# Kernel optimization log

Hardware: AMD Instinct MI355X
Metric: run time of the kernel (lower is better)

Reference implementation:

```python
import jax, jax.numpy as jnp
import numpy as np

CUTOFF = 10.0
NUM_RADIAL = 64  # RPEncoding(num_radial=64)
NHEAD = 8
D_MODEL = 512
N_SPH = 9  # lmax=2 -> 1+3+5 real spherical harmonics


def _sph_harm_l2(dirs):
    # real spherical harmonics up to l=2 on unit vectors; dirs: [..., 3]
    x, y, z = dirs[..., 0], dirs[..., 1], dirs[..., 2]
    c0 = 0.28209479177387814
    c1 = 0.4886025119029199
    c2 = 1.0925484305920792
    c20 = 0.31539156525252005
    c22 = 0.5462742152960396
    return jnp.stack([
        jnp.full_like(x, c0),
        c1 * y, c1 * z, c1 * x,
        c2 * x * y, c2 * y * z, c20 * (3.0 * z * z - 1.0), c2 * x * z,
        c22 * (x * x - y * y),
    ], axis=-1)  # [..., 9]


def _rbf(d):
    # gaussian radial basis with cosine cutoff envelope; d: [...]
    centers = jnp.linspace(0.0, CUTOFF, NUM_RADIAL)
    width = CUTOFF / NUM_RADIAL
    g = jnp.exp(-((d[..., None] - centers) ** 2) / (2.0 * width * width))
    env = 0.5 * (jnp.cos(jnp.pi * jnp.clip(d / CUTOFF, 0.0, 1.0)) + 1.0)
    return g * env[..., None]  # [..., NUM_RADIAL]


def _layer_norm(x, g, b, eps=1e-5):
    mu = jnp.mean(x, axis=-1, keepdims=True)
    var = jnp.mean(jnp.square(x - mu), axis=-1, keepdims=True)
    return (x - mu) * jax.lax.rsqrt(var + eps) * g + b


def setup_inputs() -> dict:
    key = jax.random.key(0)
    ks = jax.random.split(key, 8)
    B, L, D, F = 2, 256, D_MODEL, NUM_RADIAL * N_SPH
    src = jax.random.normal(ks[0], (B, L, D), dtype=jnp.float32)
    rel_diss = jax.random.uniform(ks[1], (B, L, L), dtype=jnp.float32) * CUTOFF
    dirs = jax.random.normal(ks[2], (B, L, L, 3), dtype=jnp.float32)
    rel_dirs = dirs / (jnp.linalg.norm(dirs, axis=-1, keepdims=True) + 1e-8)
    s = 0.02
    return {
        'src': src,
        'rel_diss': rel_diss,
        'rel_dirs': rel_dirs,
        'rp_w': jax.random.normal(ks[3], (F, D), dtype=jnp.float32) * s,
        'rp_b': jnp.zeros((D,), dtype=jnp.float32),
        'w1': jax.random.normal(ks[4], (D, 4 * D), dtype=jnp.float32) * s,
        'b1': jnp.zeros((4 * D,), dtype=jnp.float32),
        'w2': jax.random.normal(ks[5], (4 * D, D), dtype=jnp.float32) * s,
        'b2': jnp.zeros((D,), dtype=jnp.float32),
        'gamma1': jnp.ones((D,), dtype=jnp.float32),
        'beta1': jnp.zeros((D,), dtype=jnp.float32),
        'gamma2': jnp.ones((D,), dtype=jnp.float32),
        'beta2': jnp.zeros((D,), dtype=jnp.float32),
    }


def reference(src, rel_diss, rel_dirs, rp_w, rp_b, w1, b1, w2, b2,
              gamma1, beta1, gamma2, beta2):
    B, L, D = src.shape
    H, Dh = NHEAD, D // NHEAD

    # relative-position embedding: RBF(dist) outer sph-harm(dir) -> [B,L,L,576]
    rbf = _rbf(rel_diss)                 # [B,L,L,R]
    sph = _sph_harm_l2(rel_dirs)         # [B,L,L,S]
    rp_raw = (sph[..., :, None] * rbf[..., None, :]).reshape(B, L, L, -1)
    rp = jnp.einsum('blmf,fd->blmd', rp_raw, rp_w) + rp_b  # [B,L,L,D]
    rp = rp.reshape(B, L, L, H, Dh)

    # manual attention path (raw src as q/k/v, no projections, as in source)
    qh = src.reshape(B, L, H, Dh)
    rp_scores = jnp.einsum('blhd,blmhd->bhlm', qh, rp)
    base = jnp.einsum('blhd,bmhd->bhlm', qh / np.sqrt(Dh).astype(np.float32), qh)
    attn_w = jax.nn.softmax(base + rp_scores, axis=-1)
    attn = jnp.einsum('bhlm,bmhd->blhd', attn_w, qh).reshape(B, L, D)

    x = _layer_norm(src + attn, gamma1, beta1)
    h = jax.nn.leaky_relu(x @ w1 + b1, negative_slope=0.01)
    x = _layer_norm(x + h @ w2 + b2, gamma2, beta2)
    return x
```

## Files before the change

### kernel.cpp

```cpp
#include <hip/hip_runtime.h>

#define NB 2
#define NL 256
#define ND 512
#define NH 8
#define NDH 64
#define NR 64
#define NS 9
#define NF 576
#define NHS 72
#define WQROW 4608
#define RWIN 12

typedef __attribute__((ext_vector_type(8))) short bf16x8;
typedef __attribute__((ext_vector_type(4))) float f32x4;

__device__ __forceinline__ ushort f2b(float f) {
    union { float f; unsigned u; } c; c.f = f;
    unsigned u = c.u;
    return (ushort)((u + 0x7FFF + ((u >> 16) & 1)) >> 16);
}

__device__ __forceinline__ float block_sum4(float v, float* s_red) {
    #pragma unroll
    for (int off = 32; off; off >>= 1) v += __shfl_xor(v, off, 64);
    __syncthreads();
    if ((threadIdx.x & 63) == 0) s_red[threadIdx.x >> 6] = v;
    __syncthreads();
    return s_red[0] + s_red[1] + s_red[2] + s_red[3];
}

__device__ __forceinline__ float block_sum8(float v, float* s_red) {
    #pragma unroll
    for (int off = 32; off; off >>= 1) v += __shfl_xor(v, off, 64);
    __syncthreads();
    if ((threadIdx.x & 63) == 0) s_red[threadIdx.x >> 6] = v;
    __syncthreads();
    return ((s_red[0] + s_red[1]) + (s_red[2] + s_red[3])) +
           ((s_red[4] + s_red[5]) + (s_red[6] + s_red[7]));
}

__global__ __launch_bounds__(256, 4) void k_pre(const float* __restrict__ src,
                                                const float* __restrict__ rp_w,
                                                const float* __restrict__ w1,
                                                const float* __restrict__ w2,
                                                float* __restrict__ Wq,
                                                float* __restrict__ sbuf,
                                                ushort* __restrict__ w1t,
                                                ushort* __restrict__ w2t) {
    __shared__ __align__(16) char raw[26368];
    int bi = blockIdx.x;
    int t = threadIdx.x;

    if (bi < 512) {
        const float* in;
        ushort* out;
        int K, N, bx, by;
        if (bi < 256) { in = w1; out = w1t; K = 512; N = 2048; bx = bi & 31; by = bi >> 5; }
        else { int id = bi - 256; in = w2; out = w2t; K = 2048; N = 512; bx = id & 7; by = id >> 3; }
        float (*tile)[65] = (float(*)[65])raw;
        int n0 = bx * 64, k0 = by * 64;
        int r = t >> 4, c4 = (t & 15) * 4;
        #pragma unroll
        for (int i = 0; i < 4; ++i) {
            int kk = i * 16 + r;
            float4 v = *(const float4*)(in + (size_t)(k0 + kk) * N + n0 + c4);
            tile[kk][c4 + 0] = v.x;
            tile[kk][c4 + 1] = v.y;
            tile[kk][c4 + 2] = v.z;
            tile[kk][c4 + 3] = v.w;
        }
        __syncthreads();
        int rr = t >> 2, cq = (t & 3) * 16;
        ushort buf[16];
        #pragma unroll
        for (int j = 0; j < 16; ++j) buf[j] = f2b(tile[cq + j][rr]);
        ushort* op = out + (size_t)(n0 + rr) * K + k0 + cq;
        *(uint4*)(op) = *(uint4*)&buf[0];
        *(uint4*)(op + 8) = *(uint4*)&buf[8];
    } else if (bi < 1024) {
        int id = bi - 512;
        int rt = id & 63, h = id >> 6;
        float (*s_src)[64] = (float(*)[64])raw;
        float* s_B = (float*)(raw + 2048);
        int r0 = rt * 8;
        {
            int sr = t >> 5;
            int sc = (t & 31) * 2;
            *(float2*)&s_src[sr][sc] =
                *(const float2*)(src + (size_t)(r0 + sr) * ND + h * 64 + sc);
        }
        int ff = t & 63;
        int g  = t >> 6;
        int lr = t >> 2;
        int lq = t & 3;
        const float* bsrc = rp_w + h * 64;
        #pragma unroll 1
        for (int s = 0; s < NS; ++s) {
            __syncthreads();
            #pragma unroll
            for (int i = 0; i < 4; ++i) {
                int slot = i * 4 + lq;
                float4 v = *(const float4*)(bsrc + (size_t)(s * 64 + lr) * ND + slot * 4);
                int sw = slot ^ (lr & 7);
                *(float4*)&s_B[lr * 64 + sw * 4] = v;
            }
            __syncthreads();
            float a0 = 0.f, a1 = 0.f;
            #pragma unroll
            for (int d4 = 0; d4 < 16; ++d4) {
                int sw = d4 ^ (ff & 7);
                float4 bv = *(const float4*)&s_B[ff * 64 + sw * 4];
                float4 s0 = *(const float4*)&s_src[2 * g][d4 * 4];
                float4 s1 = *(const float4*)&s_src[2 * g + 1][d4 * 4];
                a0 = fmaf(bv.x, s0.x, a0);
                a0 = fmaf(bv.y, s0.y, a0);
                a0 = fmaf(bv.z, s0.z, a0);
                a0 = fmaf(bv.w, s0.w, a0);
                a1 = fmaf(bv.x, s1.x, a1);
                a1 = fmaf(bv.y, s1.y, a1);
                a1 = fmaf(bv.z, s1.z, a1);
                a1 = fmaf(bv.w, s1.w, a1);
            }
            Wq[(size_t)(r0 + 2 * g) * WQROW + ff * NHS + h * NS + s] = a0;
            Wq[(size_t)(r0 + 2 * g + 1) * WQROW + ff * NHS + h * NS + s] = a1;
        }
    } else {
        int id = bi - 1024;
        int mt = id & 3, lt = (id >> 2) & 7, bh = id >> 5;
        int b = bh >> 3, h = bh & 7;
        int m0 = mt * 64, l0 = lt * 32;
        float (*s_A)[68] = (float(*)[68])raw;
        float (*s_B)[68] = (float(*)[68])(raw + 8704);
        #pragma unroll
        for (int i = 0; i < 2; ++i) {
            int idx = i * 256 + t;
            int row = idx >> 4, c4 = idx & 15;
            float4 v = *(const float4*)(src + (size_t)(b * NL + l0 + row) * ND + h * 64 + c4 * 4);
            *(float4*)&s_A[row][c4 * 4] = v;
        }
        {
            int mr = t >> 2, qd = t & 3;
            const float* kp = src + (size_t)(b * NL + m0 + mr) * ND + h * 64 + qd * 16;
            #pragma unroll
            for (int q = 0; q < 4; ++q) {
                float4 v = *(const float4*)(kp + q * 4);
                int d = qd * 16 + q * 4;
                s_B[d + 0][mr] = v.x;
                s_B[d + 1][mr] = v.y;
                s_B[d + 2][mr] = v.z;
                s_B[d + 3][mr] = v.w;
            }
        }
        __syncthreads();
        int tx = t & 15, ty = t >> 4;
        int ty2 = ty * 2;
        float acc[2][4] = {};
        #pragma unroll
        for (int d = 0; d < 64; ++d) {
            float a0 = s_A[ty2][d];
            float a1 = s_A[ty2 + 1][d];
            float4 bv = *(const float4*)&s_B[d][tx * 4];
            acc[0][0] = fmaf(a0, bv.x, acc[0][0]);
            acc[0][1] = fmaf(a0, bv.y, acc[0][1]);
            acc[0][2] = fmaf(a0, bv.z, acc[0][2]);
            acc[0][3] = fmaf(a0, bv.w, acc[0][3]);
            acc[1][0] = fmaf(a1, bv.x, acc[1][0]);
            acc[1][1] = fmaf(a1, bv.y, acc[1][1]);
            acc[1][2] = fmaf(a1, bv.z, acc[1][2]);
            acc[1][3] = fmaf(a1, bv.w, acc[1][3]);
        }
        #pragma unroll
        for (int i = 0; i < 2; ++i) {
            size_t off = ((size_t)bh * NL + l0 + ty2 + i) * NL + m0 + tx * 4;
            *(float4*)(sbuf + off) = make_float4(acc[i][0] * 0.125f, acc[i][1] * 0.125f,
                                                 acc[i][2] * 0.125f, acc[i][3] * 0.125f);
        }
    }
}

__global__ __launch_bounds__(512, 4) void k2_fused(const float* __restrict__ src,
                                                   const float* __restrict__ rel_diss,
                                                   const float* __restrict__ rel_dirs,
                                                   const float* __restrict__ Wq,
                                                   const float* __restrict__ sbuf,
                                                   const float* __restrict__ gamma1,
                                                   const float* __restrict__ beta1,
                                                   float* __restrict__ x1buf,
                                                   ushort* __restrict__ x1bf) {
    int row = blockIdx.x;
    int b = row >> 8;
    int l = row & 255;
    int t = threadIdx.x;
    int m = t & 255;
    int hg = t >> 8;
    __shared__ float s_wq[64][76];
    __shared__ float s_l[NH][NL];
    __shared__ float s_red[8];

    const float* wrow = Wq + (size_t)row * WQROW;
    #pragma unroll
    for (int i = 0; i < 9; ++i) {
        int flat = i * 512 + t;
        int r = flat / 72, c = flat - 72 * r;
        s_wq[r][c] = wrow[flat];
    }

    float dist = rel_diss[(size_t)row * NL + m];
    const float* dirp = rel_dirs + ((size_t)row * NL + m) * 3;
    float x = dirp[0], y = dirp[1], z = dirp[2];
    float tcl = fminf(fmaxf(dist * 0.1f, 0.f), 1.f);
    float env = 0.5f * (__cosf(3.14159265358979f * tcl) + 1.f);
    int rc = (int)floorf(dist * 6.3f + 0.5f);
    int rlo = min(max(rc - 6, 0), NR - RWIN);
    float sph[NS];
    sph[0] = 0.28209479177387814f * env;
    sph[1] = 0.4886025119029199f * y * env;
    sph[2] = 0.4886025119029199f * z * env;
    sph[3] = 0.4886025119029199f * x * env;
    sph[4] = 1.0925484305920792f * x * y * env;
    sph[5] = 1.0925484305920792f * y * z * env;
    sph[6] = 0.31539156525252005f * (3.f * z * z - 1.f) * env;
    sph[7] = 1.0925484305920792f * x * z * env;
    sph[8] = 0.5462742152960396f * (x * x - y * y) * env;

    __syncthreads();

    float acc[36];
    #pragma unroll
    for (int i = 0; i < 36; ++i) acc[i] = 0.f;
    #pragma unroll 4
    for (int rw = 0; rw < RWIN; ++rw) {
        int r = rlo + rw;
        float df = dist - r * (10.f / 63.f);
        float rbf = __expf(-df * df * 20.48f);
        const float* wp = &s_wq[r][hg * 36];
        #pragma unroll
        for (int q = 0; q < 9; ++q) {
            float4 w = *(const float4*)(wp + q * 4);
            acc[q * 4 + 0] = fmaf(w.x, rbf, acc[q * 4 + 0]);
            acc[q * 4 + 1] = fmaf(w.y, rbf, acc[q * 4 + 1]);
            acc[q * 4 + 2] = fmaf(w.z, rbf, acc[q * 4 + 2]);
            acc[q * 4 + 3] = fmaf(w.w, rbf, acc[q * 4 + 3]);
        }
    }

    const float* sb = sbuf + (((size_t)(b * NH + hg * 4) * NL) + l) * NL + m;
    #pragma unroll
    for (int hh = 0; hh < 4; ++hh) {
        float sc = 0.f;
        #pragma unroll
        for (int s = 0; s < NS; ++s) sc = fmaf(sph[s], acc[hh * NS + s], sc);
        s_l[hg * 4 + hh][m] = sc + sb[(size_t)hh * NL * NL];
    }
    __syncthreads();

    int wv = t >> 6, lane = t & 63;
    {
        float v0 = s_l[wv][lane], v1 = s_l[wv][lane + 64];
        float v2 = s_l[wv][lane + 128], v3 = s_l[wv][lane + 192];
        float mx = fmaxf(fmaxf(v0, v1), fmaxf(v2, v3));
        #pragma unroll
        for (int off = 32; off; off >>= 1) mx = fmaxf(mx, __shfl_xor(mx, off, 64));
        float p0 = __expf(v0 - mx), p1 = __expf(v1 - mx);
        float p2 = __expf(v2 - mx), p3 = __expf(v3 - mx);
        float sm = p0 + p1 + p2 + p3;
        #pragma unroll
        for (int off = 32; off; off >>= 1) sm += __shfl_xor(sm, off, 64);
        float inv = 1.f / sm;
        s_l[wv][lane] = p0 * inv;
        s_l[wv][lane + 64] = p1 * inv;
        s_l[wv][lane + 128] = p2 * inv;
        s_l[wv][lane + 192] = p3 * inv;
    }
    __syncthreads();

    int d = t;
    int h0 = t >> 6;
    float a0 = 0.f, a1 = 0.f, a2 = 0.f, a3 = 0.f;
    const float* vbase = src + (size_t)b * NL * ND + d;
    #pragma unroll 2
    for (int mm = 0; mm < NL; mm += 4) {
        float4 wv4 = *(const float4*)&s_l[h0][mm];
        a0 = fmaf(wv4.x, vbase[(size_t)(mm + 0) * ND], a0);
        a1 = fmaf(wv4.y, vbase[(size_t)(mm + 1) * ND], a1);
        a2 = fmaf(wv4.z, vbase[(size_t)(mm + 2) * ND], a2);
        a3 = fmaf(wv4.w, vbase[(size_t)(mm + 3) * ND], a3);
    }
    float av = (a0 + a1) + (a2 + a3);

    float x0 = src[(size_t)row * ND + d] + av;
    float mu = block_sum8(x0, s_red) * (1.f / 512.f);
    float e0 = x0 - mu;
    float var = block_sum8(e0 * e0, s_red) * (1.f / 512.f);
    float rs = rsqrtf(var + 1e-5f);
    float o = e0 * rs * gamma1[d] + beta1[d];
    x1buf[(size_t)row * ND + d] = o;
    x1bf[(size_t)row * ND + d] = f2b(o);
}

__global__ __launch_bounds__(256) void k3_mfma(const ushort* __restrict__ A,
                                               const ushort* __restrict__ Bt,
                                               const float* __restrict__ bias,
                                               ushort* __restrict__ C) {
    const int K = 512, N = 2048;
    int n0 = blockIdx.x * 64, m0 = blockIdx.y * 64;
    int t = threadIdx.x;
    int w = t >> 6, l = t & 63;
    __shared__ ushort As[64][40];
    __shared__ ushort Bs[64][40];
    f32x4 acc0 = {0.f, 0.f, 0.f, 0.f}, acc1 = acc0, acc2 = acc0, acc3 = acc0;
    int sr = t >> 2, sq = (t & 3) * 8;
    const ushort* Ap = A + (size_t)(m0 + sr) * K + sq;
    const ushort* Bp = Bt + (size_t)(n0 + sr) * K + sq;
    int lr = l & 15, lk = (l >> 4) * 8;
    for (int k0 = 0; k0 < K; k0 += 32) {
        uint4 av = *(const uint4*)(Ap + k0);
        uint4 bv = *(const uint4*)(Bp + k0);
        __syncthreads();
        *(uint4*)&As[sr][sq] = av;
        *(uint4*)&Bs[sr][sq] = bv;
        __syncthreads();
        bf16x8 af = *(const bf16x8*)&As[w * 16 + lr][lk];
        bf16x8 b0 = *(const bf16x8*)&Bs[0 * 16 + lr][lk];
        bf16x8 b1 = *(const bf16x8*)&Bs[1 * 16 + lr][lk];
        bf16x8 b2 = *(const bf16x8*)&Bs[2 * 16 + lr][lk];
        bf16x8 b3 = *(const bf16x8*)&Bs[3 * 16 + lr][lk];
        acc0 = __builtin_amdgcn_mfma_f32_16x16x32_bf16(af, b0, acc0, 0, 0, 0);
        acc1 = __builtin_amdgcn_mfma_f32_16x16x32_bf16(af, b1, acc1, 0, 0, 0);
        acc2 = __builtin_amdgcn_mfma_f32_16x16x32_bf16(af, b2, acc2, 0, 0, 0);
        acc3 = __builtin_amdgcn_mfma_f32_16x16x32_bf16(af, b3, acc3, 0, 0, 0);
    }
    int rbase = m0 + w * 16 + (l >> 4) * 4;
    #pragma unroll
    for (int e = 0; e < 4; ++e) {
        int row = rbase + e;
        float v;
        int col0 = n0 + lr;
        v = acc0[e] + bias[col0];
        C[(size_t)row * N + col0] = f2b(v >= 0.f ? v : 0.01f * v);
        v = acc1[e] + bias[col0 + 16];
        C[(size_t)row * N + col0 + 16] = f2b(v >= 0.f ? v : 0.01f * v);
        v = acc2[e] + bias[col0 + 32];
        C[(size_t)row * N + col0 + 32] = f2b(v >= 0.f ? v : 0.01f * v);
        v = acc3[e] + bias[col0 + 48];
        C[(size_t)row * N + col0 + 48] = f2b(v >= 0.f ? v : 0.01f * v);
    }
}

__global__ __launch_bounds__(256) void k4_mfma(const ushort* __restrict__ A,
                                               const ushort* __restrict__ Bt,
                                               float* __restrict__ Cp) {
    const int K = 2048, N = 512;
    int n0 = blockIdx.x * 64, m0 = blockIdx.y * 64;
    int ks = blockIdx.z;
    int t = threadIdx.x;
    int w = t >> 6, l = t & 63;
    __shared__ ushort As[64][40];
    __shared__ ushort Bs[64][40];
    f32x4 acc0 = {0.f, 0.f, 0.f, 0.f}, acc1 = acc0, acc2 = acc0, acc3 = acc0;
    int sr = t >> 2, sq = (t & 3) * 8;
    const ushort* Ap = A + (size_t)(m0 + sr) * K + ks * 512 + sq;
    const ushort* Bp = Bt + (size_t)(n0 + sr) * K + ks * 512 + sq;
    int lr = l & 15, lk = (l >> 4) * 8;
    for (int k0 = 0; k0 < 512; k0 += 32) {
        uint4 av = *(const uint4*)(Ap + k0);
        uint4 bv = *(const uint4*)(Bp + k0);
        __syncthreads();
        *(uint4*)&As[sr][sq] = av;
        *(uint4*)&Bs[sr][sq] = bv;
        __syncthreads();
        bf16x8 af = *(const bf16x8*)&As[w * 16 + lr][lk];
        bf16x8 b0 = *(const bf16x8*)&Bs[0 * 16 + lr][lk];
        bf16x8 b1 = *(const bf16x8*)&Bs[1 * 16 + lr][lk];
        bf16x8 b2 = *(const bf16x8*)&Bs[2 * 16 + lr][lk];
        bf16x8 b3 = *(const bf16x8*)&Bs[3 * 16 + lr][lk];
        acc0 = __builtin_amdgcn_mfma_f32_16x16x32_bf16(af, b0, acc0, 0, 0, 0);
        acc1 = __builtin_amdgcn_mfma_f32_16x16x32_bf16(af, b1, acc1, 0, 0, 0);
        acc2 = __builtin_amdgcn_mfma_f32_16x16x32_bf16(af, b2, acc2, 0, 0, 0);
        acc3 = __builtin_amdgcn_mfma_f32_16x16x32_bf16(af, b3, acc3, 0, 0, 0);
    }
    float* out = Cp + ((size_t)ks << 18);
    int rbase = m0 + w * 16 + (l >> 4) * 4;
    #pragma unroll
    for (int e = 0; e < 4; ++e) {
        int row = rbase + e;
        int col0 = n0 + lr;
        out[(size_t)row * N + col0] = acc0[e];
        out[(size_t)row * N + col0 + 16] = acc1[e];
        out[(size_t)row * N + col0 + 32] = acc2[e];
        out[(size_t)row * N + col0 + 48] = acc3[e];
    }
}

__global__ __launch_bounds__(256) void k5_final(const float* __restrict__ x1buf,
                                                const float* __restrict__ zpart,
                                                const float* __restrict__ b2,
                                                const float* __restrict__ gamma2,
                                                const float* __restrict__ beta2,
                                                float* __restrict__ out) {
    int row = blockIdx.x;
    int t = threadIdx.x;
    int d0 = t * 2;
    __shared__ float s_red[8];
    size_t off = (size_t)row * ND + d0;
    float2 v = *(const float2*)(x1buf + off);
    float2 bb = *(const float2*)(b2 + d0);
    float z0 = v.x + bb.x, z1 = v.y + bb.y;
    #pragma unroll
    for (int ks = 0; ks < 4; ++ks) {
        float2 p = *(const float2*)(zpart + ((size_t)ks << 18) + off);
        z0 += p.x;
        z1 += p.y;
    }
    float mu = block_sum4(z0 + z1, s_red) * (1.f / 512.f);
    float e0 = z0 - mu, e1 = z1 - mu;
    float var = block_sum4(e0 * e0 + e1 * e1, s_red) * (1.f / 512.f);
    float rs = rsqrtf(var + 1e-5f);
    float2 g = *(const float2*)(gamma2 + d0), be = *(const float2*)(beta2 + d0);
    *(float2*)(out + off) = make_float2(e0 * rs * g.x + be.x, e1 * rs * g.y + be.y);
}

extern "C" void kernel_launch(void* const* d_in, const int* in_sizes, int n_in,
                              void* d_out, int out_size, void* d_ws, size_t ws_size,
                              hipStream_t stream) {
    const float* src      = (const float*)d_in[0];
    const float* rel_diss = (const float*)d_in[1];
    const float* rel_dirs = (const float*)d_in[2];
    const float* rp_w     = (const float*)d_in[3];
    const float* w1  = (const float*)d_in[5];
    const float* b1  = (const float*)d_in[6];
    const float* w2  = (const float*)d_in[7];
    const float* b2  = (const float*)d_in[8];
    const float* g1  = (const float*)d_in[9];
    const float* be1 = (const float*)d_in[10];
    const float* g2  = (const float*)d_in[11];
    const float* be2 = (const float*)d_in[12];
    float* out = (float*)d_out;

    float* ws = (float*)d_ws;
    float* x1buf = ws;
    float* sbuf  = x1buf + 262144;
    float* zpart = sbuf + 1048576;
    float* Wq    = zpart + 1048576;
    ushort* w1t  = (ushort*)(Wq + WQROW * 512);
    ushort* w2t  = w1t + 1048576;
    ushort* x1bf = w2t + 1048576;
    ushort* hbf  = x1bf + 262144;

    k_pre<<<1536, 256, 0, stream>>>(src, rp_w, w1, w2, Wq, sbuf, w1t, w2t);
    k2_fused<<<512, 512, 0, stream>>>(src, rel_diss, rel_dirs, Wq, sbuf,
                                      g1, be1, x1buf, x1bf);
    k3_mfma<<<dim3(32, 8), 256, 0, stream>>>(x1bf, w1t, b1, hbf);
    k4_mfma<<<dim3(8, 8, 4), 256, 0, stream>>>(hbf, w2t, zpart);
    k5_final<<<512, 256, 0, stream>>>(x1buf, zpart, b2, g2, be2, out);
}
```

Before: 66.65 us.

## Fuse final layernorm into split-K GEMM via last-block counter; vectorize PV

```diff
diff --git a/kernel.cpp b/kernel.cpp
--- a/kernel.cpp
+++ b/kernel.cpp
@@ -4,7 +4,6 @@
 #define NL 256
 #define ND 512
 #define NH 8
-#define NDH 64
 #define NR 64
 #define NS 9
 #define NF 576
@@ -19,15 +18,6 @@
     union { float f; unsigned u; } c; c.f = f;
     unsigned u = c.u;
     return (ushort)((u + 0x7FFF + ((u >> 16) & 1)) >> 16);
-}
-
-__device__ __forceinline__ float block_sum4(float v, float* s_red) {
-    #pragma unroll
-    for (int off = 32; off; off >>= 1) v += __shfl_xor(v, off, 64);
-    __syncthreads();
-    if ((threadIdx.x & 63) == 0) s_red[threadIdx.x >> 6] = v;
-    __syncthreads();
-    return s_red[0] + s_red[1] + s_red[2] + s_red[3];
 }
 
 __device__ __forceinline__ float block_sum8(float v, float* s_red) {
@@ -47,15 +37,15 @@
                                                 float* __restrict__ Wq,
                                                 float* __restrict__ sbuf,
                                                 ushort* __restrict__ w1t,
-                                                ushort* __restrict__ w2t) {
+                                                ushort* __restrict__ w2t,
+                                                unsigned* __restrict__ ctr) {
     __shared__ __align__(16) char raw[26368];
     int bi = blockIdx.x;
     int t = threadIdx.x;
+    if (bi == 0 && t < 8) ctr[t] = 0;
 
     if (bi < 512) {
-        const float* in;
-        ushort* out;
-        int K, N, bx, by;
+        const float* in; ushort* out; int K, N, bx, by;
         if (bi < 256) { in = w1; out = w1t; K = 512; N = 2048; bx = bi & 31; by = bi >> 5; }
         else { int id = bi - 256; in = w2; out = w2t; K = 2048; N = 512; bx = id & 7; by = id >> 3; }
         float (*tile)[65] = (float(*)[65])raw;
@@ -196,6 +186,7 @@
     int hg = t >> 8;
     __shared__ float s_wq[64][76];
     __shared__ float s_l[NH][NL];
+    __shared__ float s_pv[2][ND];
     __shared__ float s_red[8];
 
     const float* wrow = Wq + (size_t)row * WQROW;
@@ -205,7 +196,6 @@
         int r = flat / 72, c = flat - 72 * r;
         s_wq[r][c] = wrow[flat];
     }
-
     float dist = rel_diss[(size_t)row * NL + m];
     const float* dirp = rel_dirs + ((size_t)row * NL + m) * 3;
     float x = dirp[0], y = dirp[1], z = dirp[2];
@@ -223,7 +213,6 @@
     sph[6] = 0.31539156525252005f * (3.f * z * z - 1.f) * env;
     sph[7] = 1.0925484305920792f * x * z * env;
     sph[8] = 0.5462742152960396f * (x * x - y * y) * env;
-
     __syncthreads();
 
     float acc[36];
@@ -244,7 +233,6 @@
             acc[q * 4 + 3] = fmaf(w.w, rbf, acc[q * 4 + 3]);
         }
     }
-
     const float* sb = sbuf + (((size_t)(b * NH + hg * 4) * NL) + l) * NL + m;
     #pragma unroll
     for (int hh = 0; hh < 4; ++hh) {
@@ -275,20 +263,30 @@
     }
     __syncthreads();
 
+    {
+        int p = t & 255, half = t >> 8;
+        int d0 = p * 2;
+        int h0 = p >> 5;
+        float a0 = 0.f, a1 = 0.f, c0 = 0.f, c1 = 0.f;
+        const float* vb = src + (size_t)b * NL * ND + (size_t)(half * 128) * ND + d0;
+        const float* wl = &s_l[h0][half * 128];
+        #pragma unroll 2
+        for (int mm = 0; mm < 128; mm += 2) {
+            float2 w2v = *(const float2*)(wl + mm);
+            float2 v0 = *(const float2*)(vb + (size_t)mm * ND);
+            float2 v1 = *(const float2*)(vb + (size_t)(mm + 1) * ND);
+            a0 = fmaf(w2v.x, v0.x, a0);
+            a1 = fmaf(w2v.x, v0.y, a1);
+            c0 = fmaf(w2v.y, v1.x, c0);
+            c1 = fmaf(w2v.y, v1.y, c1);
+        }
+        s_pv[half][d0] = a0 + c0;
+        s_pv[half][d0 + 1] = a1 + c1;
+    }
+    __syncthreads();
+
     int d = t;
-    int h0 = t >> 6;
-    float a0 = 0.f, a1 = 0.f, a2 = 0.f, a3 = 0.f;
-    const float* vbase = src + (size_t)b * NL * ND + d;
-    #pragma unroll 2
-    for (int mm = 0; mm < NL; mm += 4) {
-        float4 wv4 = *(const float4*)&s_l[h0][mm];
-        a0 = fmaf(wv4.x, vbase[(size_t)(mm + 0) * ND], a0);
-        a1 = fmaf(wv4.y, vbase[(size_t)(mm + 1) * ND], a1);
-        a2 = fmaf(wv4.z, vbase[(size_t)(mm + 2) * ND], a2);
-        a3 = fmaf(wv4.w, vbase[(size_t)(mm + 3) * ND], a3);
-    }
-    float av = (a0 + a1) + (a2 + a3);
-
+    float av = s_pv[0][d] + s_pv[1][d];
     float x0 = src[(size_t)row * ND + d] + av;
     float mu = block_sum8(x0, s_red) * (1.f / 512.f);
     float e0 = x0 - mu;
@@ -323,12 +321,12 @@
         __syncthreads();
         bf16x8 af = *(const bf16x8*)&As[w * 16 + lr][lk];
         bf16x8 b0 = *(const bf16x8*)&Bs[0 * 16 + lr][lk];
-        bf16x8 b1 = *(const bf16x8*)&Bs[1 * 16 + lr][lk];
-        bf16x8 b2 = *(const bf16x8*)&Bs[2 * 16 + lr][lk];
+        bf16x8 b1v = *(const bf16x8*)&Bs[1 * 16 + lr][lk];
+        bf16x8 b2v = *(const bf16x8*)&Bs[2 * 16 + lr][lk];
         bf16x8 b3 = *(const bf16x8*)&Bs[3 * 16 + lr][lk];
         acc0 = __builtin_amdgcn_mfma_f32_16x16x32_bf16(af, b0, acc0, 0, 0, 0);
-        acc1 = __builtin_amdgcn_mfma_f32_16x16x32_bf16(af, b1, acc1, 0, 0, 0);
-        acc2 = __builtin_amdgcn_mfma_f32_16x16x32_bf16(af, b2, acc2, 0, 0, 0);
+        acc1 = __builtin_amdgcn_mfma_f32_16x16x32_bf16(af, b1v, acc1, 0, 0, 0);
+        acc2 = __builtin_amdgcn_mfma_f32_16x16x32_bf16(af, b2v, acc2, 0, 0, 0);
         acc3 = __builtin_amdgcn_mfma_f32_16x16x32_bf16(af, b3, acc3, 0, 0, 0);
     }
     int rbase = m0 + w * 16 + (l >> 4) * 4;
@@ -348,9 +346,15 @@
     }
 }
 
-__global__ __launch_bounds__(256) void k4_mfma(const ushort* __restrict__ A,
-                                               const ushort* __restrict__ Bt,
-                                               float* __restrict__ Cp) {
+__global__ __launch_bounds__(256) void k4_fused(const ushort* __restrict__ A,
+                                                const ushort* __restrict__ Bt,
+                                                float* __restrict__ Cp,
+                                                const float* __restrict__ x1buf,
+                                                const float* __restrict__ b2,
+                                                const float* __restrict__ gamma2,
+                                                const float* __restrict__ beta2,
+                                                float* __restrict__ out,
+                                                unsigned* __restrict__ ctr) {
     const int K = 2048, N = 512;
     int n0 = blockIdx.x * 64, m0 = blockIdx.y * 64;
     int ks = blockIdx.z;
@@ -358,6 +362,7 @@
     int w = t >> 6, l = t & 63;
     __shared__ ushort As[64][40];
     __shared__ ushort Bs[64][40];
+    __shared__ bool s_last;
     f32x4 acc0 = {0.f, 0.f, 0.f, 0.f}, acc1 = acc0, acc2 = acc0, acc3 = acc0;
     int sr = t >> 2, sq = (t & 3) * 8;
     const ushort* Ap = A + (size_t)(m0 + sr) * K + ks * 512 + sq;
@@ -372,53 +377,82 @@
         __syncthreads();
         bf16x8 af = *(const bf16x8*)&As[w * 16 + lr][lk];
         bf16x8 b0 = *(const bf16x8*)&Bs[0 * 16 + lr][lk];
-        bf16x8 b1 = *(const bf16x8*)&Bs[1 * 16 + lr][lk];
-        bf16x8 b2 = *(const bf16x8*)&Bs[2 * 16 + lr][lk];
+        bf16x8 b1v = *(const bf16x8*)&Bs[1 * 16 + lr][lk];
+        bf16x8 b2v = *(const bf16x8*)&Bs[2 * 16 + lr][lk];
         bf16x8 b3 = *(const bf16x8*)&Bs[3 * 16 + lr][lk];
         acc0 = __builtin_amdgcn_mfma_f32_16x16x32_bf16(af, b0, acc0, 0, 0, 0);
-        acc1 = __builtin_amdgcn_mfma_f32_16x16x32_bf16(af, b1, acc1, 0, 0, 0);
-        acc2 = __builtin_amdgcn_mfma_f32_16x16x32_bf16(af, b2, acc2, 0, 0, 0);
+        acc1 = __builtin_amdgcn_mfma_f32_16x16x32_bf16(af, b1v, acc1, 0, 0, 0);
+        acc2 = __builtin_amdgcn_mfma_f32_16x16x32_bf16(af, b2v, acc2, 0, 0, 0);
         acc3 = __builtin_amdgcn_mfma_f32_16x16x32_bf16(af, b3, acc3, 0, 0, 0);
     }
-    float* out = Cp + ((size_t)ks << 18);
-    int rbase = m0 + w * 16 + (l >> 4) * 4;
-    #pragma unroll
-    for (int e = 0; e < 4; ++e) {
-        int row = rbase + e;
-        int col0 = n0 + lr;
-        out[(size_t)row * N + col0] = acc0[e];
-        out[(size_t)row * N + col0 + 16] = acc1[e];
-        out[(size_t)row * N + col0 + 32] = acc2[e];
-        out[(size_t)row * N + col0 + 48] = acc3[e];
-    }
-}
-
-__global__ __launch_bounds__(256) void k5_final(const float* __restrict__ x1buf,
-                                                const float* __restrict__ zpart,
-                                                const float* __restrict__ b2,
-                                                const float* __restrict__ gamma2,
-                                                const float* __restrict__ beta2,
-                                                float* __restrict__ out) {
-    int row = blockIdx.x;
-    int t = threadIdx.x;
-    int d0 = t * 2;
-    __shared__ float s_red[8];
-    size_t off = (size_t)row * ND + d0;
-    float2 v = *(const float2*)(x1buf + off);
-    float2 bb = *(const float2*)(b2 + d0);
-    float z0 = v.x + bb.x, z1 = v.y + bb.y;
-    #pragma unroll
-    for (int ks = 0; ks < 4; ++ks) {
-        float2 p = *(const float2*)(zpart + ((size_t)ks << 18) + off);
-        z0 += p.x;
-        z1 += p.y;
-    }
-    float mu = block_sum4(z0 + z1, s_red) * (1.f / 512.f);
-    float e0 = z0 - mu, e1 = z1 - mu;
-    float var = block_sum4(e0 * e0 + e1 * e1, s_red) * (1.f / 512.f);
-    float rs = rsqrtf(var + 1e-5f);
-    float2 g = *(const float2*)(gamma2 + d0), be = *(const float2*)(beta2 + d0);
-    *(float2*)(out + off) = make_float2(e0 * rs * g.x + be.x, e1 * rs * g.y + be.y);
+    {
+        float* op = Cp + ((size_t)ks << 18);
+        int rbase = m0 + w * 16 + (l >> 4) * 4;
+        #pragma unroll
+        for (int e = 0; e < 4; ++e) {
+            int row = rbase + e;
+            int col0 = n0 + lr;
+            op[(size_t)row * N + col0] = acc0[e];
+            op[(size_t)row * N + col0 + 16] = acc1[e];
+            op[(size_t)row * N + col0 + 32] = acc2[e];
+            op[(size_t)row * N + col0 + 48] = acc3[e];
+        }
+    }
+    __threadfence();
+    __syncthreads();
+    if (t == 0) {
+        unsigned old = atomicAdd(&ctr[m0 >> 6], 1u);
+        s_last = (old == 31u);
+    }
+    __syncthreads();
+    if (!s_last) return;
+    __threadfence();
+
+    float4 b2a = *(const float4*)(b2 + l * 4);
+    float4 b2b = *(const float4*)(b2 + 256 + l * 4);
+    float4 g2a = *(const float4*)(gamma2 + l * 4);
+    float4 g2b = *(const float4*)(gamma2 + 256 + l * 4);
+    float4 bea = *(const float4*)(beta2 + l * 4);
+    float4 beb = *(const float4*)(beta2 + 256 + l * 4);
+    #pragma unroll 2
+    for (int i = 0; i < 16; ++i) {
+        int row = m0 + w * 16 + i;
+        size_t base = (size_t)row * ND;
+        float4 xA = *(const float4*)(x1buf + base + l * 4);
+        float4 xB = *(const float4*)(x1buf + base + 256 + l * 4);
+        float z0 = xA.x + b2a.x, z1 = xA.y + b2a.y, z2 = xA.z + b2a.z, z3 = xA.w + b2a.w;
+        float z4 = xB.x + b2b.x, z5 = xB.y + b2b.y, z6 = xB.z + b2b.z, z7 = xB.w + b2b.w;
+        #pragma unroll
+        for (int k = 0; k < 4; ++k) {
+            const float* zp = Cp + ((size_t)k << 18) + base;
+            float4 pA = *(const float4*)(zp + l * 4);
+            float4 pB = *(const float4*)(zp + 256 + l * 4);
+            z0 += pA.x; z1 += pA.y; z2 += pA.z; z3 += pA.w;
+            z4 += pB.x; z5 += pB.y; z6 += pB.z; z7 += pB.w;
+        }
+        float s1 = ((z0 + z1) + (z2 + z3)) + ((z4 + z5) + (z6 + z7));
+        #pragma unroll
+        for (int off = 32; off; off >>= 1) s1 += __shfl_xor(s1, off, 64);
+        float mu = s1 * (1.f / 512.f);
+        float e0 = z0 - mu, e1 = z1 - mu, e2 = z2 - mu, e3 = z3 - mu;
+        float e4 = z4 - mu, e5 = z5 - mu, e6 = z6 - mu, e7 = z7 - mu;
+        float s2 = ((e0 * e0 + e1 * e1) + (e2 * e2 + e3 * e3)) +
+                   ((e4 * e4 + e5 * e5) + (e6 * e6 + e7 * e7));
+        #pragma unroll
+        for (int off = 32; off; off >>= 1) s2 += __shfl_xor(s2, off, 64);
+        float rs = rsqrtf(s2 * (1.f / 512.f) + 1e-5f);
+        float4 oA, oB;
+        oA.x = e0 * rs * g2a.x + bea.x;
+        oA.y = e1 * rs * g2a.y + bea.y;
+        oA.z = e2 * rs * g2a.z + bea.z;
+        oA.w = e3 * rs * g2a.w + bea.w;
+        oB.x = e4 * rs * g2b.x + beb.x;
+        oB.y = e5 * rs * g2b.y + beb.y;
+        oB.z = e6 * rs * g2b.z + beb.z;
+        oB.w = e7 * rs * g2b.w + beb.w;
+        *(float4*)(out + base + l * 4) = oA;
+        *(float4*)(out + base + 256 + l * 4) = oB;
+    }
 }
 
 extern "C" void kernel_launch(void* const* d_in, const int* in_sizes, int n_in,
@@ -447,11 +481,12 @@
     ushort* w2t  = w1t + 1048576;
     ushort* x1bf = w2t + 1048576;
     ushort* hbf  = x1bf + 262144;
-
-    k_pre<<<1536, 256, 0, stream>>>(src, rp_w, w1, w2, Wq, sbuf, w1t, w2t);
+    unsigned* ctr = (unsigned*)(hbf + 1048576);
+
+    k_pre<<<1536, 256, 0, stream>>>(src, rp_w, w1, w2, Wq, sbuf, w1t, w2t, ctr);
     k2_fused<<<512, 512, 0, stream>>>(src, rel_diss, rel_dirs, Wq, sbuf,
                                       g1, be1, x1buf, x1bf);
     k3_mfma<<<dim3(32, 8), 256, 0, stream>>>(x1bf, w1t, b1, hbf);
-    k4_mfma<<<dim3(8, 8, 4), 256, 0, stream>>>(hbf, w2t, zpart);
-    k5_final<<<512, 256, 0, stream>>>(x1buf, zpart, b2, g2, be2, out);
-}
+    k4_fused<<<dim3(8, 8, 4), 256, 0, stream>>>(hbf, w2t, zpart,
+                                                x1buf, b2, g2, be2, out, ctr);
+}
```

New measurement: 111.2 us. 1.67x slower.
